# Kernel tuning notes

Measured on AMD Instinct MI355X. Metric: run time of the kernel, lower is better.

Reference implementation:

```python
import jax, jax.numpy as jnp
import numpy as np

N = 100_000      # nodes
E = 1_600_000    # directed edges (avg degree 16)
F_IN = 128       # num_node_features
H = 8            # heads in conv1
C = 32           # hidden_channels
G = 64           # graphs in batch
NC = 10          # num_classes


def setup_inputs() -> dict:
    key = jax.random.key(0)
    ks = jax.random.split(key, 12)
    gl = lambda k, shape, fan: (jax.random.normal(k, shape, jnp.float32) / np.sqrt(fan)).astype(jnp.float32)
    return {
        "x": jax.random.normal(ks[0], (N, F_IN), jnp.float32),
        "edge_index": jax.random.randint(ks[1], (2, E), 0, N, dtype=jnp.int32),
        "batch": jnp.sort(jax.random.randint(ks[2], (N,), 0, G, dtype=jnp.int32)),
        "W1": gl(ks[3], (F_IN, H * C), F_IN),
        "att_src1": gl(ks[4], (H, C), C),
        "att_dst1": gl(ks[5], (H, C), C),
        "b1": jnp.zeros((H * C,), jnp.float32),
        "W2": gl(ks[6], (H * C, C), H * C),
        "att_src2": gl(ks[7], (1, C), C),
        "att_dst2": gl(ks[8], (1, C), C),
        "b2": jnp.zeros((C,), jnp.float32),
        "Wlin": gl(ks[9], (C, NC), C),
        "blin": jnp.zeros((NC,), jnp.float32),
    }


def gat_conv(x, src, dst, W, att_src, att_dst, bias, heads, ch, concat):
    """PyG GATConv (eval mode): gather, LeakyReLU(0.2) scores, segment softmax over dst, scatter-sum."""
    n = x.shape[0]
    h = (x @ W).reshape(n, heads, ch)                     # [N,H,C]
    a_s = jnp.sum(h * att_src, axis=-1)                   # [N,H]
    a_d = jnp.sum(h * att_dst, axis=-1)                   # [N,H]
    e = jax.nn.leaky_relu(a_s[src] + a_d[dst], 0.2)       # [E,H]
    m = jax.ops.segment_max(e, dst, num_segments=n)       # [N,H], stable softmax
    p = jnp.exp(e - m[dst])
    z = jax.ops.segment_sum(p, dst, num_segments=n)
    coef = p / (z[dst] + 1e-16)                           # [E,H]
    out = jax.ops.segment_sum(coef[:, :, None] * h[src], dst, num_segments=n)  # [N,H,C]
    out = out.reshape(n, heads * ch) if concat else out.mean(axis=1)
    return out + bias


def reference(x, edge_index, batch, W1, att_src1, att_dst1, b1,
              W2, att_src2, att_dst2, b2, Wlin, blin):
    n = x.shape[0]
    loops = jnp.arange(n, dtype=edge_index.dtype)         # GATConv add_self_loops=True
    src = jnp.concatenate([edge_index[0], loops])
    dst = jnp.concatenate([edge_index[1], loops])

    h = gat_conv(x, src, dst, W1, att_src1, att_dst1, b1, H, C, concat=True)
    h = jax.nn.elu(h)                                     # dropout is identity in eval
    h = gat_conv(h, src, dst, W2, att_src2, att_dst2, b2, 1, C, concat=False)

    # global_mean_pool over graph ids
    sums = jax.ops.segment_sum(h, batch, num_segments=G)  # [G,C]
    cnts = jax.ops.segment_sum(jnp.ones((n,), h.dtype), batch, num_segments=G)
    pooled = sums / jnp.maximum(cnts, 1.0)[:, None]

    return pooled @ Wlin + blin                           # [G,NC]
```

## Files before the change

### kernel.cpp

```cpp
#include <hip/hip_runtime.h>
#include <cstdint>

#define NN 100000
#define EE 1600000
#define GG 64
#define FIN 128
#define HC 256
#define NC 10

typedef short v8s __attribute__((ext_vector_type(8)));
typedef float v4f __attribute__((ext_vector_type(4)));

static __device__ __forceinline__ float lrelu(float x) { return x > 0.f ? x : 0.2f * x; }
static __device__ __forceinline__ float bf2f(unsigned short b) {
  return __uint_as_float(((unsigned int)b) << 16);
}
static __device__ __forceinline__ unsigned short f2bf(float f) {
  unsigned int u = __float_as_uint(f);
  unsigned int r = (u + 0x7FFFu + ((u >> 16) & 1u)) >> 16;
  return (unsigned short)r;
}
static __device__ __forceinline__ void unpack2(unsigned int u, float& f0, float& f1) {
  f0 = __uint_as_float(u << 16);
  f1 = __uint_as_float(u & 0xFFFF0000u);
}

__global__ __launch_bounds__(256) void k_prepx(const float* __restrict__ x,
                                               unsigned short* __restrict__ xb,
                                               unsigned int* __restrict__ counts) {
  const int idx = blockIdx.x * 256 + threadIdx.x;
  const int i4 = idx * 4;
  float4 v = *(const float4*)(x + i4);
  ushort4 u;
  u.x = f2bf(v.x); u.y = f2bf(v.y); u.z = f2bf(v.z); u.w = f2bf(v.w);
  *(ushort4*)(xb + i4) = u;
  if (idx < NN) counts[idx] = 0u;
}

__global__ void k_prep(const float* __restrict__ W1, unsigned short* __restrict__ W1tg) {
  const int b = blockIdx.x, t = threadIdx.x;
  if (t < 128) W1tg[b * 128 + t] = f2bf(W1[t * HC + b]);
}

__global__ void k_prepw2(const float* __restrict__ W2,
                         unsigned short* __restrict__ W2thi,
                         unsigned short* __restrict__ W2tlo) {
  const int b = blockIdx.x;
  const int t = threadIdx.x;
  float w = W2[t * 32 + b];
  unsigned short hi = f2bf(w);
  W2thi[b * 256 + t] = hi;
  W2tlo[b * 256 + t] = f2bf(w - bf2f(hi));
}

__global__ __launch_bounds__(256) void k_gemm1(const unsigned short* __restrict__ xb,
                                               const unsigned short* __restrict__ W1tg,
                                               const float* __restrict__ att_src1,
                                               const float* __restrict__ att_dst1,
                                               unsigned short* __restrict__ h1b,
                                               float* __restrict__ as1,
                                               float* __restrict__ ad1) {
  const int t = threadIdx.x;
  const int m0 = blockIdx.x * 64;
  const int n0 = blockIdx.y * 128;
  const int hb = blockIdx.y * 4;
  const int lane = t & 63;
  const int wm = t >> 6;
  const int ml = lane & 15;
  const int quad = lane >> 4;
  int row = m0 + wm * 16 + ml; if (row >= NN) row = NN - 1;
  v4f acc[8];
#pragma unroll
  for (int tt = 0; tt < 8; ++tt) acc[tt] = (v4f){0.f, 0.f, 0.f, 0.f};
#pragma unroll
  for (int kk = 0; kk < 4; ++kk) {
    const int k0 = kk * 32 + quad * 8;
    v8s a = *(const v8s*)(xb + (size_t)row * FIN + k0);
#pragma unroll
    for (int tt = 0; tt < 8; ++tt) {
      v8s b = *(const v8s*)(W1tg + (size_t)(n0 + tt * 16 + ml) * FIN + k0);
      acc[tt] = __builtin_amdgcn_mfma_f32_16x16x32_bf16(a, b, acc[tt], 0, 0, 0);
    }
  }
#pragma unroll
  for (int tt = 0; tt < 8; ++tt) {
#pragma unroll
    for (int r = 0; r < 4; ++r) {
      int rg = m0 + wm * 16 + quad * 4 + r;
      if (rg < NN) h1b[(size_t)rg * HC + n0 + tt * 16 + ml] = f2bf(acc[tt][r]);
    }
  }
  float ps[4][4], pd[4][4];
#pragma unroll
  for (int i = 0; i < 4; ++i)
#pragma unroll
    for (int r = 0; r < 4; ++r) { ps[i][r] = 0.f; pd[i][r] = 0.f; }
#pragma unroll
  for (int i = 0; i < 4; ++i) {
#pragma unroll
    for (int half = 0; half < 2; ++half) {
      const int tt = 2 * i + half;
      const float a_s = att_src1[(hb + i) * 32 + half * 16 + ml];
      const float a_d = att_dst1[(hb + i) * 32 + half * 16 + ml];
#pragma unroll
      for (int r = 0; r < 4; ++r) {
        ps[i][r] += acc[tt][r] * a_s;
        pd[i][r] += acc[tt][r] * a_d;
      }
    }
  }
#pragma unroll
  for (int i = 0; i < 4; ++i) {
#pragma unroll
    for (int r = 0; r < 4; ++r) {
      float s = ps[i][r], d = pd[i][r];
      s += __shfl_xor(s, 1, 64); s += __shfl_xor(s, 2, 64);
      s += __shfl_xor(s, 4, 64); s += __shfl_xor(s, 8, 64);
      d += __shfl_xor(d, 1, 64); d += __shfl_xor(d, 2, 64);
      d += __shfl_xor(d, 4, 64); d += __shfl_xor(d, 8, 64);
      ps[i][r] = s; pd[i][r] = d;
    }
  }
  if (ml == 0) {
#pragma unroll
    for (int r = 0; r < 4; ++r) {
      int rg = m0 + wm * 16 + quad * 4 + r;
      if (rg < NN) {
#pragma unroll
        for (int i = 0; i < 4; ++i) {
          as1[rg * 8 + hb + i] = ps[i][r];
          ad1[rg * 8 + hb + i] = pd[i][r];
        }
      }
    }
  }
}

__global__ void k_count(const int* __restrict__ ei, int* __restrict__ counts) {
  int e = blockIdx.x * 256 + threadIdx.x;
  if (e < EE) atomicAdd(&counts[ei[EE + e]], 1);
}

__global__ void k_scan1(const int* __restrict__ counts, int* __restrict__ offs,
                        int* __restrict__ bsums) {
  __shared__ int s[256];
  const int t = threadIdx.x;
  const int i = blockIdx.x * 256 + t;
  int v = (i < NN) ? counts[i] : 0;
  s[t] = v;
  __syncthreads();
  for (int off = 1; off < 256; off <<= 1) {
    int tv = (t >= off) ? s[t - off] : 0;
    __syncthreads();
    s[t] += tv;
    __syncthreads();
  }
  if (i < NN) offs[i] = s[t] - v;
  if (t == 255) bsums[blockIdx.x] = s[255];
}

__global__ void k_scan2(int* __restrict__ bsums, int nb) {
  __shared__ int s[512];
  const int t = threadIdx.x;
  int v = (t < nb) ? bsums[t] : 0;
  s[t] = v;
  __syncthreads();
  for (int off = 1; off < 512; off <<= 1) {
    int tv = (t >= off) ? s[t - off] : 0;
    __syncthreads();
    s[t] += tv;
    __syncthreads();
  }
  if (t < nb) bsums[t] = s[t] - v;
}

__global__ void k_scan3(int* __restrict__ offs, const int* __restrict__ bsums,
                        int* __restrict__ cursor) {
  const int i = blockIdx.x * 256 + threadIdx.x;
  if (i < NN) {
    int v = offs[i] + bsums[i >> 8];
    offs[i] = v;
    cursor[i] = v;
  }
  if (i == 0) offs[NN] = EE;
}

__global__ void k_scatter(const int* __restrict__ ei, int* __restrict__ cursor,
                          int* __restrict__ esrc) {
  int e = blockIdx.x * 256 + threadIdx.x;
  if (e < EE) {
    int s = ei[e];
    int d = ei[EE + e];
    int p = atomicAdd(&cursor[d], 1);
    esrc[p] = s;
  }
}

__global__ __launch_bounds__(256) void k_agg1(const unsigned short* __restrict__ h1b,
                                              const float* __restrict__ as1,
                                              const float* __restrict__ ad1,
                                              const int* __restrict__ offs,
                                              const int* __restrict__ esrc,
                                              const float* __restrict__ b1,
                                              const unsigned short* __restrict__ W2thi,
                                              const unsigned short* __restrict__ W2tlo,
                                              const float* __restrict__ att_src2,
                                              const float* __restrict__ att_dst2,
                                              unsigned short* __restrict__ h2b,
                                              float* __restrict__ as2,
                                              float* __restrict__ ad2) {
  __shared__ __attribute__((aligned(16))) unsigned short o1hi[4][256];
  __shared__ __attribute__((aligned(16))) unsigned short o1lo[4][256];
  const int t = threadIdx.x;
  const int lane = t & 63;
  const int w = t >> 6;
  const int n0 = blockIdx.x * 4;
  const int n = n0 + w;
  const int head = lane >> 3;
  const uint2* __restrict__ h1u2 = (const uint2*)h1b;
  const int start = offs[n], end = offs[n + 1];
  const float adn = ad1[n * 8 + head];

  float z, a0, a1, a2, a3;
  {
    float w0 = __expf(lrelu(as1[n * 8 + head] + adn));
    uint2 q = h1u2[(size_t)n * 64 + lane];
    float f0, f1, f2, f3; unpack2(q.x, f0, f1); unpack2(q.y, f2, f3);
    z = w0; a0 = w0 * f0; a1 = w0 * f1; a2 = w0 * f2; a3 = w0 * f3;
  }
  for (int base = start; base < end; base += 64) {
    const int cnt = min(64, end - base);
    int sreg = 0;
    if (lane < cnt) sreg = esrc[base + lane];
#pragma unroll 8
    for (int j = 0; j < cnt; ++j) {
      const int sj = __builtin_amdgcn_readlane(sreg, j);
      const float sc = as1[sj * 8 + head];
      const uint2 q = h1u2[(size_t)sj * 64 + lane];
      const float wv = __expf(lrelu(sc + adn));
      float f0, f1, f2, f3; unpack2(q.x, f0, f1); unpack2(q.y, f2, f3);
      z += wv;
      a0 += wv * f0; a1 += wv * f1; a2 += wv * f2; a3 += wv * f3;
    }
  }
  {
    const float zi = 1.0f / (z + 1e-16f);
    const float4 bb = *(const float4*)(b1 + 4 * lane);
    float v0 = a0 * zi + bb.x;
    float v1 = a1 * zi + bb.y;
    float v2 = a2 * zi + bb.z;
    float v3 = a3 * zi + bb.w;
    v0 = v0 > 0.f ? v0 : (__expf(v0) - 1.0f);
    v1 = v1 > 0.f ? v1 : (__expf(v1) - 1.0f);
    v2 = v2 > 0.f ? v2 : (__expf(v2) - 1.0f);
    v3 = v3 > 0.f ? v3 : (__expf(v3) - 1.0f);
    ushort4 hh, ll;
    hh.x = f2bf(v0); hh.y = f2bf(v1); hh.z = f2bf(v2); hh.w = f2bf(v3);
    ll.x = f2bf(v0 - bf2f(hh.x));
    ll.y = f2bf(v1 - bf2f(hh.y));
    ll.z = f2bf(v2 - bf2f(hh.z));
    ll.w = f2bf(v3 - bf2f(hh.w));
    *(ushort4*)&o1hi[w][4 * lane] = hh;
    *(ushort4*)&o1lo[w][4 * lane] = ll;
  }
  __syncthreads();
  if (w == 0) {
    const int ml = lane & 15;
    const int quad = lane >> 4;
    const int mr = ml & 3;
    v4f acc[2];
    acc[0] = (v4f){0.f, 0.f, 0.f, 0.f};
    acc[1] = (v4f){0.f, 0.f, 0.f, 0.f};
#pragma unroll
    for (int kk = 0; kk < 8; ++kk) {
      const int k0 = kk * 32 + quad * 8;
      v8s ah = *(const v8s*)&o1hi[mr][k0];
      v8s al = *(const v8s*)&o1lo[mr][k0];
#pragma unroll
      for (int tt = 0; tt < 2; ++tt) {
        v8s bh = *(const v8s*)(W2thi + (size_t)(tt * 16 + ml) * 256 + k0);
        v8s bl = *(const v8s*)(W2tlo + (size_t)(tt * 16 + ml) * 256 + k0);
        acc[tt] = __builtin_amdgcn_mfma_f32_16x16x32_bf16(ah, bh, acc[tt], 0, 0, 0);
        acc[tt] = __builtin_amdgcn_mfma_f32_16x16x32_bf16(al, bh, acc[tt], 0, 0, 0);
        acc[tt] = __builtin_amdgcn_mfma_f32_16x16x32_bf16(ah, bl, acc[tt], 0, 0, 0);
      }
    }
    if (quad == 0) {
      const float s0 = att_src2[ml], s1 = att_src2[16 + ml];
      const float d0 = att_dst2[ml], d1 = att_dst2[16 + ml];
#pragma unroll
      for (int r = 0; r < 4; ++r) {
        const int nn = n0 + r;
        const float h0 = acc[0][r], h1v = acc[1][r];
        h2b[(size_t)nn * 32 + ml] = f2bf(h0);
        h2b[(size_t)nn * 32 + 16 + ml] = f2bf(h1v);
        float ps = h0 * s0 + h1v * s1;
        float pd = h0 * d0 + h1v * d1;
        ps += __shfl_xor(ps, 1, 64); ps += __shfl_xor(ps, 2, 64);
        ps += __shfl_xor(ps, 4, 64); ps += __shfl_xor(ps, 8, 64);
        pd += __shfl_xor(pd, 1, 64); pd += __shfl_xor(pd, 2, 64);
        pd += __shfl_xor(pd, 4, 64); pd += __shfl_xor(pd, 8, 64);
        if (ml == 0) { as2[nn] = ps; ad2[nn] = pd; }
      }
    }
  }
}

__global__ __launch_bounds__(256) void k_agg2(const unsigned short* __restrict__ h2b,
                                              const float* __restrict__ as2,
                                              const float* __restrict__ ad2,
                                              const int* __restrict__ offs,
                                              const int* __restrict__ esrc,
                                              const float* __restrict__ b2,
                                              float* __restrict__ h3) {
  const int t = threadIdx.x;
  const int lane = t & 63;
  const int wv = t >> 6;
  const int n = blockIdx.x * 4 + wv;
  const int col = lane & 15;
  const int slot = lane >> 4;
  const unsigned int* h2u = (const unsigned int*)h2b;
  const int start = offs[n], end = offs[n + 1];
  const float adn = ad2[n];
  float z = 0.f, acc0 = 0.f, acc1 = 0.f;
  if (slot == 0) {
    float w0 = __expf(lrelu(as2[n] + adn));
    unsigned int q = h2u[(size_t)n * 16 + col];
    float f0, f1; unpack2(q, f0, f1);
    z = w0; acc0 = w0 * f0; acc1 = w0 * f1;
  }
  for (int base = start; base < end; base += 64) {
    const int cnt = min(64, end - base);
    int sreg = 0; float wreg = 0.f;
    if (lane < cnt) {
      sreg = esrc[base + lane];
      wreg = __expf(lrelu(as2[sreg] + adn));
    }
    const int jmax = (cnt + 3) >> 2;
#pragma unroll 4
    for (int j = 0; j < jmax; ++j) {
      const int e = 4 * j + slot;
      int sj = __shfl(sreg, e, 64);
      float wj = __shfl(wreg, e, 64);
      if (e < cnt) {
        unsigned int q = h2u[(size_t)sj * 16 + col];
        float f0, f1; unpack2(q, f0, f1);
        z += wj; acc0 += wj * f0; acc1 += wj * f1;
      }
    }
  }
  acc0 += __shfl_xor(acc0, 16, 64); acc0 += __shfl_xor(acc0, 32, 64);
  acc1 += __shfl_xor(acc1, 16, 64); acc1 += __shfl_xor(acc1, 32, 64);
  z    += __shfl_xor(z, 16, 64);    z    += __shfl_xor(z, 32, 64);
  if (slot == 0) {
    const float zi = 1.0f / (z + 1e-16f);
    float2 bb = *(const float2*)(b2 + 2 * col);
    float2 o;
    o.x = acc0 * zi + bb.x;
    o.y = acc1 * zi + bb.y;
    *(float2*)(h3 + (size_t)n * 32 + 2 * col) = o;
  }
}

__global__ __launch_bounds__(256) void k_poolfin(const float* __restrict__ h3,
                                                 const int* __restrict__ batch,
                                                 const float* __restrict__ Wlin,
                                                 const float* __restrict__ blin,
                                                 float* __restrict__ out) {
  __shared__ int bounds[2];
  __shared__ float red[8][33];
  __shared__ float mean[32];
  const int g = blockIdx.x;
  const int t = threadIdx.x;
  if (t < 2) {
    int target = g + t;
    int lo = 0, hi = NN;
    while (lo < hi) { int mid = (lo + hi) >> 1; if (batch[mid] < target) lo = mid + 1; else hi = mid; }
    bounds[t] = lo;
  }
  __syncthreads();
  const int lo = bounds[0], hi = bounds[1];
  const int rr = t >> 5, c = t & 31;
  float a = 0.f;
  for (int r = lo + rr; r < hi; r += 8) a += h3[(size_t)r * 32 + c];
  red[rr][c] = a;
  __syncthreads();
  if (rr == 0) {
    float s = 0.f;
#pragma unroll
    for (int i = 0; i < 8; ++i) s += red[i][c];
    float ct = (float)(hi - lo);
    ct = ct > 1.f ? ct : 1.f;
    mean[c] = s / ct;
  }
  __syncthreads();
  if (t < NC) {
    float acc = 0.f;
#pragma unroll
    for (int cc = 0; cc < 32; ++cc) acc += mean[cc] * Wlin[cc * NC + t];
    out[g * NC + t] = acc + blin[t];
  }
}

extern "C" void kernel_launch(void* const* d_in, const int* in_sizes, int n_in,
                              void* d_out, int out_size, void* d_ws, size_t ws_size,
                              hipStream_t stream) {
  const float* x        = (const float*)d_in[0];
  const int*   ei       = (const int*)d_in[1];
  const int*   batch    = (const int*)d_in[2];
  const float* W1       = (const float*)d_in[3];
  const float* att_src1 = (const float*)d_in[4];
  const float* att_dst1 = (const float*)d_in[5];
  const float* b1       = (const float*)d_in[6];
  const float* W2       = (const float*)d_in[7];
  const float* att_src2 = (const float*)d_in[8];
  const float* att_dst2 = (const float*)d_in[9];
  const float* b2       = (const float*)d_in[10];
  const float* Wlin     = (const float*)d_in[11];
  const float* blin     = (const float*)d_in[12];
  float* out = (float*)d_out;
  char* ws = (char*)d_ws;

  unsigned short* h1b   = (unsigned short*)(ws + 0);
  unsigned short* xb    = (unsigned short*)(ws + 51200000);
  float* h3     = (float*)(ws + 51200000);
  float* as1    = (float*)(ws + 76800000);
  float* ad1    = (float*)(ws + 80000000);
  int* counts   = (int*)(ws + 83200000);
  int* offs     = (int*)(ws + 83600000);
  int* cursor   = (int*)(ws + 84000256);
  int* esrc     = (int*)(ws + 84400256);
  int* bsums    = (int*)(ws + 90800256);
  unsigned short* h2b   = (unsigned short*)(ws + 90802304);
  float* as2    = (float*)(ws + 97202304);
  float* ad2    = (float*)(ws + 97602304);
  unsigned short* W1tg  = (unsigned short*)(ws + 98002304);
  unsigned short* W2thi = (unsigned short*)(ws + 98067840);
  unsigned short* W2tlo = (unsigned short*)(ws + 98084224);

  const int nb_scan = (NN + 255) / 256;

  k_prepx<<<12500, 256, 0, stream>>>(x, xb, (unsigned int*)counts);
  k_prep<<<256, 128, 0, stream>>>(W1, W1tg);
  k_prepw2<<<32, 256, 0, stream>>>(W2, W2thi, W2tlo);

  dim3 g1((NN + 63) / 64, 2);
  k_gemm1<<<g1, 256, 0, stream>>>(xb, W1tg, att_src1, att_dst1, h1b, as1, ad1);

  k_count<<<(EE + 255) / 256, 256, 0, stream>>>(ei, counts);
  k_scan1<<<nb_scan, 256, 0, stream>>>(counts, offs, bsums);
  k_scan2<<<1, 512, 0, stream>>>(bsums, nb_scan);
  k_scan3<<<nb_scan, 256, 0, stream>>>(offs, bsums, cursor);
  k_scatter<<<(EE + 255) / 256, 256, 0, stream>>>(ei, cursor, esrc);

  k_agg1<<<NN / 4, 256, 0, stream>>>(h1b, as1, ad1, offs, esrc, b1, W2thi, W2tlo,
                                     att_src2, att_dst2, h2b, as2, ad2);

  k_agg2<<<NN / 4, 256, 0, stream>>>(h2b, as2, ad2, offs, esrc, b2, h3);
  k_poolfin<<<GG, 256, 0, stream>>>(h3, batch, Wlin, blin, out);
}
```

Baseline: 670.0 us.

## Precompute per-edge attention weights in LDS and fuse degree count into prep

In the first aggregation, each lane now computes all 8 head attention weights for one edge and stages them in shared memory. The inner gather loop then reads four weights at once instead of doing a per-edge scalar load and exp in every lane. The second aggregation stages source index and weight pairs in LDS instead of using two shuffles per edge, and drops the bounds check. Edge degree counting moves into the x-conversion kernel after a memset, removing one launch. Risks: the unrolled-by-4 loop reads past cnt, which relies on weights padded with zeros, and it issues gathers for indices padded with zeros.

```diff
diff --git a/kernel.cpp b/kernel.cpp
--- a/kernel.cpp
+++ b/kernel.cpp
@@ -27,14 +27,15 @@
 
 __global__ __launch_bounds__(256) void k_prepx(const float* __restrict__ x,
                                                unsigned short* __restrict__ xb,
-                                               unsigned int* __restrict__ counts) {
+                                               const int* __restrict__ ei,
+                                               int* __restrict__ counts) {
   const int idx = blockIdx.x * 256 + threadIdx.x;
   const int i4 = idx * 4;
   float4 v = *(const float4*)(x + i4);
   ushort4 u;
   u.x = f2bf(v.x); u.y = f2bf(v.y); u.z = f2bf(v.z); u.w = f2bf(v.w);
   *(ushort4*)(xb + i4) = u;
-  if (idx < NN) counts[idx] = 0u;
+  if (idx < EE) atomicAdd(&counts[ei[EE + idx]], 1);
 }
 
 __global__ void k_prep(const float* __restrict__ W1, unsigned short* __restrict__ W1tg) {
@@ -134,11 +135,6 @@
       }
     }
   }
-}
-
-__global__ void k_count(const int* __restrict__ ei, int* __restrict__ counts) {
-  int e = blockIdx.x * 256 + threadIdx.x;
-  if (e < EE) atomicAdd(&counts[ei[EE + e]], 1);
 }
 
 __global__ void k_scan1(const int* __restrict__ counts, int* __restrict__ offs,
@@ -209,8 +205,9 @@
                                               unsigned short* __restrict__ h2b,
                                               float* __restrict__ as2,
                                               float* __restrict__ ad2) {
-  __shared__ __attribute__((aligned(16))) unsigned short o1hi[4][256];
-  __shared__ __attribute__((aligned(16))) unsigned short o1lo[4][256];
+  __shared__ float wl[4][8][68];
+  __shared__ __attribute__((aligned(16))) unsigned short o1hi[4][264];
+  __shared__ __attribute__((aligned(16))) unsigned short o1lo[4][264];
   const int t = threadIdx.x;
   const int lane = t & 63;
   const int w = t >> 6;
@@ -219,28 +216,61 @@
   const int head = lane >> 3;
   const uint2* __restrict__ h1u2 = (const uint2*)h1b;
   const int start = offs[n], end = offs[n + 1];
-  const float adn = ad1[n * 8 + head];
+
+  const float4 dnA = *(const float4*)(ad1 + n * 8);
+  const float4 dnB = *(const float4*)(ad1 + n * 8 + 4);
+  const float adnh = head < 4 ? (head == 0 ? dnA.x : head == 1 ? dnA.y : head == 2 ? dnA.z : dnA.w)
+                              : (head == 4 ? dnB.x : head == 5 ? dnB.y : head == 6 ? dnB.z : dnB.w);
 
   float z, a0, a1, a2, a3;
   {
-    float w0 = __expf(lrelu(as1[n * 8 + head] + adn));
+    float w0 = __expf(lrelu(as1[n * 8 + head] + adnh));
     uint2 q = h1u2[(size_t)n * 64 + lane];
     float f0, f1, f2, f3; unpack2(q.x, f0, f1); unpack2(q.y, f2, f3);
     z = w0; a0 = w0 * f0; a1 = w0 * f1; a2 = w0 * f2; a3 = w0 * f3;
   }
   for (int base = start; base < end; base += 64) {
     const int cnt = min(64, end - base);
-    int sreg = 0;
-    if (lane < cnt) sreg = esrc[base + lane];
-#pragma unroll 8
-    for (int j = 0; j < cnt; ++j) {
-      const int sj = __builtin_amdgcn_readlane(sreg, j);
-      const float sc = as1[sj * 8 + head];
-      const uint2 q = h1u2[(size_t)sj * 64 + lane];
-      const float wv = __expf(lrelu(sc + adn));
-      float f0, f1, f2, f3; unpack2(q.x, f0, f1); unpack2(q.y, f2, f3);
-      z += wv;
-      a0 += wv * f0; a1 += wv * f1; a2 += wv * f2; a3 += wv * f3;
+    int s = 0;
+    if (lane < cnt) s = esrc[base + lane];
+    const float4 avA = *(const float4*)(as1 + (size_t)s * 8);
+    const float4 avB = *(const float4*)(as1 + (size_t)s * 8 + 4);
+    float wv8[8];
+    wv8[0] = __expf(lrelu(avA.x + dnA.x)); wv8[1] = __expf(lrelu(avA.y + dnA.y));
+    wv8[2] = __expf(lrelu(avA.z + dnA.z)); wv8[3] = __expf(lrelu(avA.w + dnA.w));
+    wv8[4] = __expf(lrelu(avB.x + dnB.x)); wv8[5] = __expf(lrelu(avB.y + dnB.y));
+    wv8[6] = __expf(lrelu(avB.z + dnB.z)); wv8[7] = __expf(lrelu(avB.w + dnB.w));
+    const bool act = lane < cnt;
+#pragma unroll
+    for (int h = 0; h < 8; ++h) wl[w][h][lane] = act ? wv8[h] : 0.f;
+#pragma unroll 2
+    for (int jb = 0; jb < cnt; jb += 4) {
+      const float4 wq = *(const float4*)&wl[w][head][jb];
+      z += wq.x + wq.y + wq.z + wq.w;
+      {
+        const int sj = __builtin_amdgcn_readlane(s, jb);
+        const uint2 q = h1u2[(size_t)sj * 64 + lane];
+        float f0, f1, f2, f3; unpack2(q.x, f0, f1); unpack2(q.y, f2, f3);
+        a0 += wq.x * f0; a1 += wq.x * f1; a2 += wq.x * f2; a3 += wq.x * f3;
+      }
+      {
+        const int sj = __builtin_amdgcn_readlane(s, jb + 1);
+        const uint2 q = h1u2[(size_t)sj * 64 + lane];
+        float f0, f1, f2, f3; unpack2(q.x, f0, f1); unpack2(q.y, f2, f3);
+        a0 += wq.y * f0; a1 += wq.y * f1; a2 += wq.y * f2; a3 += wq.y * f3;
+      }
+      {
+        const int sj = __builtin_amdgcn_readlane(s, jb + 2);
+        const uint2 q = h1u2[(size_t)sj * 64 + lane];
+        float f0, f1, f2, f3; unpack2(q.x, f0, f1); unpack2(q.y, f2, f3);
+        a0 += wq.z * f0; a1 += wq.z * f1; a2 += wq.z * f2; a3 += wq.z * f3;
+      }
+      {
+        const int sj = __builtin_amdgcn_readlane(s, jb + 3);
+        const uint2 q = h1u2[(size_t)sj * 64 + lane];
+        float f0, f1, f2, f3; unpack2(q.x, f0, f1); unpack2(q.y, f2, f3);
+        a0 += wq.w * f0; a1 += wq.w * f1; a2 += wq.w * f2; a3 += wq.w * f3;
+      }
     }
   }
   {
@@ -313,40 +343,40 @@
                                               const int* __restrict__ esrc,
                                               const float* __restrict__ b2,
                                               float* __restrict__ h3) {
+  __shared__ int2 swl[4][64];
   const int t = threadIdx.x;
   const int lane = t & 63;
   const int wv = t >> 6;
   const int n = blockIdx.x * 4 + wv;
   const int col = lane & 15;
   const int slot = lane >> 4;
-  const unsigned int* h2u = (const unsigned int*)h2b;
+  const unsigned int* __restrict__ h2u = (const unsigned int*)h2b;
   const int start = offs[n], end = offs[n + 1];
   const float adn = ad2[n];
   float z = 0.f, acc0 = 0.f, acc1 = 0.f;
   if (slot == 0) {
     float w0 = __expf(lrelu(as2[n] + adn));
-    unsigned int q = h2u[(size_t)n * 16 + col];
+    unsigned int q = h2u[(unsigned)(n * 16 + col)];
     float f0, f1; unpack2(q, f0, f1);
     z = w0; acc0 = w0 * f0; acc1 = w0 * f1;
   }
   for (int base = start; base < end; base += 64) {
     const int cnt = min(64, end - base);
-    int sreg = 0; float wreg = 0.f;
+    int s = 0; float wgt = 0.f;
     if (lane < cnt) {
-      sreg = esrc[base + lane];
-      wreg = __expf(lrelu(as2[sreg] + adn));
-    }
+      s = esrc[base + lane];
+      wgt = __expf(lrelu(as2[s] + adn));
+    }
+    swl[wv][lane] = make_int2(s, __float_as_int(wgt));
     const int jmax = (cnt + 3) >> 2;
 #pragma unroll 4
     for (int j = 0; j < jmax; ++j) {
-      const int e = 4 * j + slot;
-      int sj = __shfl(sreg, e, 64);
-      float wj = __shfl(wreg, e, 64);
-      if (e < cnt) {
-        unsigned int q = h2u[(size_t)sj * 16 + col];
-        float f0, f1; unpack2(q, f0, f1);
-        z += wj; acc0 += wj * f0; acc1 += wj * f1;
-      }
+      const int2 p = swl[wv][4 * j + slot];
+      const int sj = p.x;
+      const float wj = __int_as_float(p.y);
+      unsigned int q = h2u[(unsigned)(sj * 16 + col)];
+      float f0, f1; unpack2(q, f0, f1);
+      z += wj; acc0 += wj * f0; acc1 += wj * f1;
     }
   }
   acc0 += __shfl_xor(acc0, 16, 64); acc0 += __shfl_xor(acc0, 32, 64);
@@ -440,14 +470,14 @@
 
   const int nb_scan = (NN + 255) / 256;
 
-  k_prepx<<<12500, 256, 0, stream>>>(x, xb, (unsigned int*)counts);
+  hipMemsetAsync(counts, 0, NN * sizeof(int), stream);
+  k_prepx<<<12500, 256, 0, stream>>>(x, xb, ei, counts);
   k_prep<<<256, 128, 0, stream>>>(W1, W1tg);
   k_prepw2<<<32, 256, 0, stream>>>(W2, W2thi, W2tlo);
 
   dim3 g1((NN + 63) / 64, 2);
   k_gemm1<<<g1, 256, 0, stream>>>(xb, W1tg, att_src1, att_dst1, h1b, as1, ad1);
 
-  k_count<<<(EE + 255) / 256, 256, 0, stream>>>(ei, counts);
   k_scan1<<<nb_scan, 256, 0, stream>>>(counts, offs, bsums);
   k_scan2<<<1, 512, 0, stream>>>(bsums, nb_scan);
   k_scan3<<<nb_scan, 256, 0, stream>>>(offs, bsums, cursor);
```

Measured after the change: 636.0 us. 1.05x faster.
